# Kernel tuning notes

Measured on AMD Instinct MI355X. Metric: run time of the kernel, lower is better.

The kernel has to match this reference:

```python
import jax, jax.numpy as jnp
import numpy as np

D_MODEL = 1024
NHEAD = 16
HEAD_DIM = D_MODEL // NHEAD


def setup_inputs() -> dict:
    key = jax.random.key(0)
    k1, k2, k3 = jax.random.split(key, 3)
    x = jax.random.normal(k1, (4, 2048, D_MODEL), dtype=jnp.float32)
    # xavier_uniform init for weights, zero bias
    lim_qkv = float(np.sqrt(6.0 / (D_MODEL + 3 * D_MODEL)))
    w_qkv = jax.random.uniform(k2, (3 * D_MODEL, D_MODEL), jnp.float32, -lim_qkv, lim_qkv)
    b_qkv = jnp.zeros((3 * D_MODEL,), jnp.float32)
    lim_o = float(np.sqrt(6.0 / (D_MODEL + D_MODEL)))
    w_o = jax.random.uniform(k3, (D_MODEL, D_MODEL), jnp.float32, -lim_o, lim_o)
    b_o = jnp.zeros((D_MODEL,), jnp.float32)
    return {"x": x, "w_qkv": w_qkv, "b_qkv": b_qkv, "w_o": w_o, "b_o": b_o}


def reference(x, w_qkv, b_qkv, w_o, b_o):
    B, S, _ = x.shape
    qkv = x @ w_qkv.T + b_qkv                      # [B,S,3D]
    qkv = qkv.reshape(B, S, NHEAD, 3 * HEAD_DIM).transpose(0, 2, 1, 3)  # [B,H,S,3d]
    q, k, v = jnp.split(qkv, 3, axis=-1)           # each [B,H,S,d]
    scale = 1.0 / jnp.sqrt(jnp.asarray(HEAD_DIM, x.dtype))
    logits = jnp.einsum('bhqd,bhkd->bhqk', q, k) * scale
    attn = jax.nn.softmax(logits, axis=-1)
    vals = jnp.einsum('bhqk,bhkd->bhqd', attn, v)  # [B,H,S,d]
    vals = vals.transpose(0, 2, 1, 3).reshape(B, S, D_MODEL)
    return vals @ w_o.T + b_o
```

## Files before the change

kernel.cpp:

```cpp
#include <hip/hip_runtime.h>
#include <hip/hip_bf16.h>
#include <stdint.h>

typedef unsigned short u16;
typedef __bf16 bf16x8 __attribute__((ext_vector_type(8)));
typedef short s16x4 __attribute__((ext_vector_type(4)));
typedef float f32x4 __attribute__((ext_vector_type(4)));
typedef u16 u16x4v __attribute__((ext_vector_type(4)));

#define AS1 __attribute__((address_space(1)))
#define AS3 __attribute__((address_space(3)))

__device__ __forceinline__ void gld_lds16(const u16* g, u16* l) {
    __builtin_amdgcn_global_load_lds((const AS1 uint32_t*)g, (AS3 uint32_t*)l, 16, 0, 0);
}

__device__ __forceinline__ u16 f2bf(float f) {
    union { float f; uint32_t u; } v; v.f = f;
    uint32_t u = v.u;
    return (u16)((u + 0x7FFFu + ((u >> 16) & 1u)) >> 16);
}

#define QSCALE 0.18033688011112042f

__global__ void cast_f32_bf16(const float* __restrict__ in, u16* __restrict__ out, int n4) {
    int i = blockIdx.x * blockDim.x + threadIdx.x;
    if (i < n4) {
        float4 f = ((const float4*)in)[i];
        u16x4v o;
        o.x = f2bf(f.x); o.y = f2bf(f.y); o.z = f2bf(f.z); o.w = f2bf(f.w);
        ((u16x4v*)out)[i] = o;
    }
}

template <int MODE>
__global__ __launch_bounds__(256, 2) void gemm_bt(
    const u16* __restrict__ A, const u16* __restrict__ B,
    const float* __restrict__ bias, float* __restrict__ Cf,
    u16* __restrict__ qb, u16* __restrict__ kb, u16* __restrict__ vT,
    int K, int ldc)
{
    __shared__ __align__(16) u16 As[128 * 32];
    __shared__ __align__(16) u16 Bs[128 * 32];
    const int tid = threadIdx.x;
    const int lane = tid & 63;
    const int w = tid >> 6;
    const int wm = (w >> 1) << 6;
    const int wn = (w & 1) << 6;
    const int r = lane & 15;
    const int q = lane >> 4;
    const int m0 = blockIdx.y << 7;
    const int n0 = blockIdx.x << 7;

    const f32x4 zero4 = {0.f, 0.f, 0.f, 0.f};
    f32x4 acc[4][4];
#pragma unroll
    for (int i = 0; i < 4; ++i)
#pragma unroll
        for (int j = 0; j < 4; ++j) acc[i][j] = zero4;

    const int nk = K >> 5;
    for (int kt = 0; kt < nk; ++kt) {
        const int kk = kt << 5;
#pragma unroll
        for (int p = 0; p < 2; ++p) {
            const int idx = (p << 8) + tid;
            const int row = idx >> 2;
            const int cg = ((idx & 3) - (row >> 1)) & 3;
            gld_lds16(A + (m0 + row) * K + kk + (cg << 3), &As[idx << 3]);
            gld_lds16(B + (n0 + row) * K + kk + (cg << 3), &Bs[idx << 3]);
        }
        __syncthreads();
        bf16x8 af[4], bf[4];
#pragma unroll
        for (int i = 0; i < 4; ++i) {
            const int ra = wm + (i << 4) + r;
            af[i] = *(const bf16x8*)&As[((ra << 2) + ((q + (ra >> 1)) & 3)) << 3];
            const int rb = wn + (i << 4) + r;
            bf[i] = *(const bf16x8*)&Bs[((rb << 2) + ((q + (rb >> 1)) & 3)) << 3];
        }
#pragma unroll
        for (int i = 0; i < 4; ++i)
#pragma unroll
            for (int j = 0; j < 4; ++j)
                acc[i][j] = __builtin_amdgcn_mfma_f32_16x16x32_bf16(af[i], bf[j], acc[i][j], 0, 0, 0);
        __syncthreads();
    }

#pragma unroll
    for (int j = 0; j < 4; ++j) {
        const int col = n0 + wn + (j << 4) + r;
        const float bv = bias[col];
        if (MODE == 0) {
#pragma unroll
            for (int i = 0; i < 4; ++i)
#pragma unroll
                for (int ii = 0; ii < 4; ++ii) {
                    const int rowg = m0 + wm + (i << 4) + (q << 2) + ii;
                    Cf[rowg * ldc + col] = acc[i][j][ii] + bv;
                }
        } else {
            const int c0 = n0 + wn + (j << 4);
            const int h = c0 / 192;
            const int rem = c0 - h * 192;
            const int region = rem >> 6;
            const int colp = (h << 6) + (rem - (region << 6)) + r;
            if (region == 0) {
#pragma unroll
                for (int i = 0; i < 4; ++i)
#pragma unroll
                    for (int ii = 0; ii < 4; ++ii) {
                        const int rowg = m0 + wm + (i << 4) + (q << 2) + ii;
                        qb[rowg * 1024 + colp] = f2bf((acc[i][j][ii] + bv) * QSCALE);
                    }
            } else if (region == 1) {
#pragma unroll
                for (int i = 0; i < 4; ++i)
#pragma unroll
                    for (int ii = 0; ii < 4; ++ii) {
                        const int rowg = m0 + wm + (i << 4) + (q << 2) + ii;
                        kb[rowg * 1024 + colp] = f2bf(acc[i][j][ii] + bv);
                    }
            } else {
#pragma unroll
                for (int i = 0; i < 4; ++i) {
                    const int rowg0 = m0 + wm + (i << 4) + (q << 2);
                    u16x4v vv;
                    vv.x = f2bf(acc[i][j][0] + bv);
                    vv.y = f2bf(acc[i][j][1] + bv);
                    vv.z = f2bf(acc[i][j][2] + bv);
                    vv.w = f2bf(acc[i][j][3] + bv);
                    *(u16x4v*)&vT[(size_t)colp * 8192 + rowg0] = vv;
                }
            }
        }
    }
}

__device__ __forceinline__ void stage_kv(
    const u16* __restrict__ kb, const u16* __restrict__ vT, u16* __restrict__ KV,
    int tid, int h, size_t rowbase, int k0)
{
#pragma unroll
    for (int p = 0; p < 2; ++p) {
        const int idx = (p << 8) + tid;
        const int row = idx >> 3;
        const int cg = ((idx & 7) - row) & 7;
        gld_lds16(kb + (rowbase + k0 + row) * 1024 + (h << 6) + (cg << 3), &KV[idx << 3]);
    }
#pragma unroll
    for (int p = 0; p < 2; ++p) {
        const int idx = (p << 8) + tid;
        const int hd = idx >> 3;
        const int pc = idx & 7;
        const int lc = (pc - hd - (hd >> 3)) & 7;
        gld_lds16(vT + (size_t)((h << 6) + hd) * 8192 + rowbase + k0 + (lc << 3),
                  &KV[4096 + (idx << 3)]);
    }
}

__global__ __launch_bounds__(256, 3) void attn(
    const u16* __restrict__ qb, const u16* __restrict__ kb,
    const u16* __restrict__ vT, u16* __restrict__ vals)
{
    __shared__ __align__(16) u16 S[16384];

    const int tid = threadIdx.x;
    const int lane = tid & 63;
    const int w = tid >> 6;
    const int r = lane & 15;
    const int q = lane >> 4;
    const int h = blockIdx.x;
    const int q0 = blockIdx.y << 7;
    const int b = blockIdx.z;
    const size_t rowbase = (size_t)b * 2048;

#pragma unroll
    for (int p = 0; p < 4; ++p) {
        const int idx = (p << 8) + tid;
        const int row = idx >> 3;
        const int cg = ((idx & 7) - row) & 7;
        gld_lds16(qb + (rowbase + q0 + row) * 1024 + (h << 6) + (cg << 3), &S[idx << 3]);
    }
    stage_kv(kb, vT, S + 8192, tid, h, rowbase, 0);
    __syncthreads();

    bf16x8 bq[2][2];
#pragma unroll
    for (int ks = 0; ks < 2; ++ks) {
        const int L = (ks << 2) + q;
#pragma unroll
        for (int nt = 0; nt < 2; ++nt) {
            const int row = (w << 5) + (nt << 4) + r;
            bq[ks][nt] = *(const bf16x8*)&S[(row << 6) + (((L + row) & 7) << 3)];
        }
    }
    __syncthreads();

    const f32x4 zero4 = {0.f, 0.f, 0.f, 0.f};
    f32x4 oacc[4][2];
    f32x4 lacc[2];
#pragma unroll
    for (int ht = 0; ht < 4; ++ht)
#pragma unroll
        for (int nt = 0; nt < 2; ++nt) oacc[ht][nt] = zero4;
    lacc[0] = zero4; lacc[1] = zero4;

    const s16x4 ones = {0x3F80, 0x3F80, 0x3F80, 0x3F80};

    for (int kt = 0; kt < 32; ++kt) {
        const int cur = kt & 1;
        if (kt > 0) __syncthreads();
        u16* bufP = (cur == 0) ? (S + 0) : (S + 8192);
        const u16* bufC = (cur == 0) ? (S + 8192) : (S + 0);
        if (kt < 31) stage_kv(kb, vT, bufP, tid, h, rowbase, (kt + 1) << 6);
        const u16* Ks = bufC;
        const u16* VTs = bufC + 4096;

        f32x4 sacc[4][2];
#pragma unroll
        for (int mt = 0; mt < 4; ++mt)
#pragma unroll
            for (int nt = 0; nt < 2; ++nt) sacc[mt][nt] = zero4;
#pragma unroll
        for (int ks = 0; ks < 2; ++ks) {
            const int L = (ks << 2) + q;
            bf16x8 ak[4];
#pragma unroll
            for (int mt = 0; mt < 4; ++mt) {
                const int row = (mt << 4) + r;
                ak[mt] = *(const bf16x8*)&Ks[(row << 6) + (((L + row) & 7) << 3)];
            }
#pragma unroll
            for (int mt = 0; mt < 4; ++mt)
#pragma unroll
                for (int nt = 0; nt < 2; ++nt)
                    sacc[mt][nt] = __builtin_amdgcn_mfma_f32_16x16x32_bf16(ak[mt], bq[ks][nt], sacc[mt][nt], 0, 0, 0);
        }

        s16x4 pb[4][2];
#pragma unroll
        for (int mt = 0; mt < 4; ++mt) {
#pragma unroll
            for (int nt = 0; nt < 2; ++nt) {
                const float e0 = __builtin_amdgcn_exp2f(sacc[mt][nt][0]);
                const float e1 = __builtin_amdgcn_exp2f(sacc[mt][nt][1]);
                const float e2 = __builtin_amdgcn_exp2f(sacc[mt][nt][2]);
                const float e3 = __builtin_amdgcn_exp2f(sacc[mt][nt][3]);
                union { __hip_bfloat162 h2[2]; s16x4 v; } u;
                u.h2[0] = __float22bfloat162_rn(float2{e0, e1});
                u.h2[1] = __float22bfloat162_rn(float2{e2, e3});
                pb[mt][nt] = u.v;
                lacc[nt] = __builtin_amdgcn_mfma_f32_16x16x16bf16_1k(ones, pb[mt][nt], lacc[nt], 0, 0, 0);
            }
        }

#pragma unroll
        for (int mt = 0; mt < 4; ++mt) {
            s16x4 av[4];
#pragma unroll
            for (int ht = 0; ht < 4; ++ht) {
                const int hd = (ht << 4) + r;
                const int chunk = (mt << 1) + (q >> 1);
                const int pc = (chunk + hd + (hd >> 3)) & 7;
                av[ht] = *(const s16x4*)&VTs[(hd << 6) + (pc << 3) + ((q & 1) << 2)];
            }
#pragma unroll
            for (int ht = 0; ht < 4; ++ht)
#pragma unroll
                for (int nt = 0; nt < 2; ++nt)
                    oacc[ht][nt] = __builtin_amdgcn_mfma_f32_16x16x16bf16_1k(av[ht], pb[mt][nt], oacc[ht][nt], 0, 0, 0);
        }
    }

#pragma unroll
    for (int nt = 0; nt < 2; ++nt) {
        const float inv = 1.f / lacc[nt][0];
        const int srow = q0 + (w << 5) + (nt << 4) + r;
#pragma unroll
        for (int ht = 0; ht < 4; ++ht) {
            u16x4v vv;
            vv.x = f2bf(oacc[ht][nt][0] * inv);
            vv.y = f2bf(oacc[ht][nt][1] * inv);
            vv.z = f2bf(oacc[ht][nt][2] * inv);
            vv.w = f2bf(oacc[ht][nt][3] * inv);
            const int col = (h << 6) + (ht << 4) + (q << 2);
            *(u16x4v*)&vals[(rowbase + srow) * 1024 + col] = vv;
        }
    }
}

extern "C" void kernel_launch(void* const* d_in, const int* in_sizes, int n_in,
                              void* d_out, int out_size, void* d_ws, size_t ws_size,
                              hipStream_t stream) {
    (void)in_sizes; (void)n_in; (void)out_size; (void)ws_size;
    const float* x     = (const float*)d_in[0];
    const float* w_qkv = (const float*)d_in[1];
    const float* b_qkv = (const float*)d_in[2];
    const float* w_o   = (const float*)d_in[3];
    const float* b_o   = (const float*)d_in[4];
    float* out = (float*)d_out;

    char* ws = (char*)d_ws;
    u16* xb    = (u16*)(ws);
    u16* wqkvb = (u16*)(ws + (size_t)(16 << 20));
    u16* wob   = (u16*)(ws + (size_t)(22 << 20));
    u16* qb    = (u16*)(ws + (size_t)(24 << 20));
    u16* kb    = (u16*)(ws + (size_t)(40 << 20));
    u16* vTb   = (u16*)(ws + (size_t)(56 << 20));
    u16* valsb = (u16*)(ws + (size_t)(72 << 20));

    cast_f32_bf16<<<8192, 256, 0, stream>>>(x, xb, 2097152);
    cast_f32_bf16<<<3072, 256, 0, stream>>>(w_qkv, wqkvb, 786432);
    cast_f32_bf16<<<1024, 256, 0, stream>>>(w_o, wob, 262144);

    gemm_bt<1><<<dim3(24, 64), 256, 0, stream>>>(xb, wqkvb, b_qkv, nullptr,
                                                 qb, kb, vTb, 1024, 3072);

    attn<<<dim3(16, 16, 4), 256, 0, stream>>>(qb, kb, vTb, valsb);

    gemm_bt<0><<<dim3(8, 64), 256, 0, stream>>>(valsb, wob, b_o, out,
                                                nullptr, nullptr, nullptr, 1024, 1024);
}
```

Baseline: 278.0 us.

## Switch attention to 32x32x16 MFMA with permlane32 swap and XOR-swizzled LDS

Rewrites the attention inner loop to use 32x32x16 bf16 MFMA tiles instead of 16x16 tiles. The exponentiated scores are repacked into the B-operand layout with v_permlane32_swap, so they feed the PV MFMA straight from registers. The change also swaps the additive LDS swizzle for an XOR swizzle with precomputed staging pointers, and wraps the MFMA blocks in s_setprio. The aim is fewer MFMA issues, fewer LDS reads and less address arithmetic per tile. The cost is higher register pressure and a dependency on the MI355 permlane32_swap instruction.

New measurement: 291.3 us. 1.05x slower.

```diff
diff --git a/kernel.cpp b/kernel.cpp
--- a/kernel.cpp
+++ b/kernel.cpp
@@ -3,10 +3,12 @@
 #include <stdint.h>
 
 typedef unsigned short u16;
+typedef uint32_t u32;
 typedef __bf16 bf16x8 __attribute__((ext_vector_type(8)));
-typedef short s16x4 __attribute__((ext_vector_type(4)));
 typedef float f32x4 __attribute__((ext_vector_type(4)));
+typedef float f32x16 __attribute__((ext_vector_type(16)));
 typedef u16 u16x4v __attribute__((ext_vector_type(4)));
+typedef u32 u32x2 __attribute__((ext_vector_type(2)));
 
 #define AS1 __attribute__((address_space(1)))
 #define AS3 __attribute__((address_space(3)))
@@ -19,6 +21,15 @@
     union { float f; uint32_t u; } v; v.f = f;
     uint32_t u = v.u;
     return (u16)((u + 0x7FFFu + ((u >> 16) & 1u)) >> 16);
+}
+
+__device__ __forceinline__ u32x2 pl32swap(u32 a, u32 b) {
+#if __has_builtin(__builtin_amdgcn_permlane32_swap)
+    return __builtin_amdgcn_permlane32_swap(a, b, false, false);
+#else
+    asm volatile("v_permlane32_swap_b32 %0, %1" : "+v"(a), "+v"(b));
+    u32x2 r; r[0] = a; r[1] = b; return r;
+#endif
 }
 
 #define QSCALE 0.18033688011112042f
@@ -137,157 +148,149 @@
     }
 }
 
-__device__ __forceinline__ void stage_kv(
-    const u16* __restrict__ kb, const u16* __restrict__ vT, u16* __restrict__ KV,
-    int tid, int h, size_t rowbase, int k0)
-{
-#pragma unroll
-    for (int p = 0; p < 2; ++p) {
-        const int idx = (p << 8) + tid;
-        const int row = idx >> 3;
-        const int cg = ((idx & 7) - row) & 7;
-        gld_lds16(kb + (rowbase + k0 + row) * 1024 + (h << 6) + (cg << 3), &KV[idx << 3]);
-    }
-#pragma unroll
-    for (int p = 0; p < 2; ++p) {
-        const int idx = (p << 8) + tid;
-        const int hd = idx >> 3;
-        const int pc = idx & 7;
-        const int lc = (pc - hd - (hd >> 3)) & 7;
-        gld_lds16(vT + (size_t)((h << 6) + hd) * 8192 + rowbase + k0 + (lc << 3),
-                  &KV[4096 + (idx << 3)]);
-    }
-}
-
 __global__ __launch_bounds__(256, 3) void attn(
     const u16* __restrict__ qb, const u16* __restrict__ kb,
     const u16* __restrict__ vT, u16* __restrict__ vals)
 {
     __shared__ __align__(16) u16 S[16384];
 
-    const int tid = threadIdx.x;
+    const int tid  = threadIdx.x;
     const int lane = tid & 63;
-    const int w = tid >> 6;
-    const int r = lane & 15;
-    const int q = lane >> 4;
-    const int h = blockIdx.x;
-    const int q0 = blockIdx.y << 7;
-    const int b = blockIdx.z;
+    const int w    = tid >> 6;
+    const int c    = lane & 31;
+    const int h2   = lane >> 5;
+    const int head = blockIdx.x;
+    const int q0   = blockIdx.y << 7;
+    const int b    = blockIdx.z;
     const size_t rowbase = (size_t)b * 2048;
 
 #pragma unroll
     for (int p = 0; p < 4; ++p) {
         const int idx = (p << 8) + tid;
         const int row = idx >> 3;
-        const int cg = ((idx & 7) - row) & 7;
-        gld_lds16(qb + (rowbase + q0 + row) * 1024 + (h << 6) + (cg << 3), &S[idx << 3]);
-    }
-    stage_kv(kb, vT, S + 8192, tid, h, rowbase, 0);
+        const int cg  = (idx & 7) ^ (row & 7);
+        gld_lds16(qb + (rowbase + q0 + row) * 1024 + (head << 6) + (cg << 3), &S[idx << 3]);
+    }
+
+    const int srow8 = tid >> 3;
+    const int scg   = (tid & 7) ^ (srow8 & 7);
+    const u16* gK = kb + (rowbase + srow8) * 1024 + (head << 6) + (scg << 3);
+    const u16* gV = vT + (size_t)((head << 6) + srow8) * 8192 + rowbase + (scg << 3);
+
+    {
+        u16* buf = S + 8192;
+        gld_lds16(gK,             &buf[tid << 3]);
+        gld_lds16(gK + 32 * 1024, &buf[2048 + (tid << 3)]);
+        gld_lds16(gV,             &buf[4096 + (tid << 3)]);
+        gld_lds16(gV + 32 * 8192, &buf[6144 + (tid << 3)]);
+    }
     __syncthreads();
 
-    bf16x8 bq[2][2];
-#pragma unroll
-    for (int ks = 0; ks < 2; ++ks) {
-        const int L = (ks << 2) + q;
-#pragma unroll
-        for (int nt = 0; nt < 2; ++nt) {
-            const int row = (w << 5) + (nt << 4) + r;
-            bq[ks][nt] = *(const bf16x8*)&S[(row << 6) + (((L + row) & 7) << 3)];
-        }
+    const int qrow = (w << 5) + c;
+    bf16x8 bq[4];
+#pragma unroll
+    for (int dc = 0; dc < 4; ++dc) {
+        const int L = (dc << 1) + h2;
+        bq[dc] = *(const bf16x8*)&S[(qrow << 6) + ((L ^ (c & 7)) << 3)];
     }
     __syncthreads();
 
-    const f32x4 zero4 = {0.f, 0.f, 0.f, 0.f};
-    f32x4 oacc[4][2];
-    f32x4 lacc[2];
-#pragma unroll
-    for (int ht = 0; ht < 4; ++ht)
-#pragma unroll
-        for (int nt = 0; nt < 2; ++nt) oacc[ht][nt] = zero4;
-    lacc[0] = zero4; lacc[1] = zero4;
-
-    const s16x4 ones = {0x3F80, 0x3F80, 0x3F80, 0x3F80};
+    const int ldsb = (c << 6) + ((h2 ^ (c & 7)) << 3);
+
+    f32x16 oacc[2], lacc;
+#pragma unroll
+    for (int i = 0; i < 16; ++i) { oacc[0][i] = 0.f; oacc[1][i] = 0.f; lacc[i] = 0.f; }
+
+    union { u16 u[8]; bf16x8 v; } Ou;
+#pragma unroll
+    for (int i = 0; i < 8; ++i) Ou.u[i] = 0x3F80;
+    const bf16x8 ones8 = Ou.v;
+
+    const u16* gKr = gK + 65536;
+    const u16* gVr = gV + 64;
 
     for (int kt = 0; kt < 32; ++kt) {
         const int cur = kt & 1;
         if (kt > 0) __syncthreads();
         u16* bufP = (cur == 0) ? (S + 0) : (S + 8192);
         const u16* bufC = (cur == 0) ? (S + 8192) : (S + 0);
-        if (kt < 31) stage_kv(kb, vT, bufP, tid, h, rowbase, (kt + 1) << 6);
-        const u16* Ks = bufC;
+        if (kt < 31) {
+            gld_lds16(gKr,             &bufP[tid << 3]);
+            gld_lds16(gKr + 32 * 1024, &bufP[2048 + (tid << 3)]);
+            gld_lds16(gVr,             &bufP[4096 + (tid << 3)]);
+            gld_lds16(gVr + 32 * 8192, &bufP[6144 + (tid << 3)]);
+            gKr += 65536;
+            gVr += 64;
+        }
+        const u16* Ks  = bufC;
         const u16* VTs = bufC + 4096;
 
-        f32x4 sacc[4][2];
-#pragma unroll
-        for (int mt = 0; mt < 4; ++mt)
-#pragma unroll
-            for (int nt = 0; nt < 2; ++nt) sacc[mt][nt] = zero4;
-#pragma unroll
-        for (int ks = 0; ks < 2; ++ks) {
-            const int L = (ks << 2) + q;
-            bf16x8 ak[4];
-#pragma unroll
-            for (int mt = 0; mt < 4; ++mt) {
-                const int row = (mt << 4) + r;
-                ak[mt] = *(const bf16x8*)&Ks[(row << 6) + (((L + row) & 7) << 3)];
+        f32x16 sacc[2];
+#pragma unroll
+        for (int i = 0; i < 16; ++i) { sacc[0][i] = 0.f; sacc[1][i] = 0.f; }
+        __builtin_amdgcn_s_setprio(1);
+#pragma unroll
+        for (int mt = 0; mt < 2; ++mt)
+#pragma unroll
+            for (int dc = 0; dc < 4; ++dc) {
+                const bf16x8 ak = *(const bf16x8*)&Ks[ldsb ^ ((mt << 11) | (dc << 4))];
+                sacc[mt] = __builtin_amdgcn_mfma_f32_32x32x16_bf16(ak, bq[dc], sacc[mt], 0, 0, 0);
             }
-#pragma unroll
-            for (int mt = 0; mt < 4; ++mt)
-#pragma unroll
-                for (int nt = 0; nt < 2; ++nt)
-                    sacc[mt][nt] = __builtin_amdgcn_mfma_f32_16x16x32_bf16(ak[mt], bq[ks][nt], sacc[mt][nt], 0, 0, 0);
-        }
-
-        s16x4 pb[4][2];
-#pragma unroll
-        for (int mt = 0; mt < 4; ++mt) {
-#pragma unroll
-            for (int nt = 0; nt < 2; ++nt) {
-                const float e0 = __builtin_amdgcn_exp2f(sacc[mt][nt][0]);
-                const float e1 = __builtin_amdgcn_exp2f(sacc[mt][nt][1]);
-                const float e2 = __builtin_amdgcn_exp2f(sacc[mt][nt][2]);
-                const float e3 = __builtin_amdgcn_exp2f(sacc[mt][nt][3]);
-                union { __hip_bfloat162 h2[2]; s16x4 v; } u;
-                u.h2[0] = __float22bfloat162_rn(float2{e0, e1});
-                u.h2[1] = __float22bfloat162_rn(float2{e2, e3});
-                pb[mt][nt] = u.v;
-                lacc[nt] = __builtin_amdgcn_mfma_f32_16x16x16bf16_1k(ones, pb[mt][nt], lacc[nt], 0, 0, 0);
+        __builtin_amdgcn_s_setprio(0);
+
+#pragma unroll
+        for (int mt = 0; mt < 2; ++mt) {
+            bf16x8 av[4];
+#pragma unroll
+            for (int ht = 0; ht < 2; ++ht)
+#pragma unroll
+                for (int c16 = 0; c16 < 2; ++c16)
+                    av[(ht << 1) | c16] =
+                        *(const bf16x8*)&VTs[ldsb ^ ((ht << 11) | (mt << 5) | (c16 << 4))];
+
+            u32 pk[8];
+#pragma unroll
+            for (int p = 0; p < 8; ++p) {
+                const float e0 = __builtin_amdgcn_exp2f(sacc[mt][2 * p]);
+                const float e1 = __builtin_amdgcn_exp2f(sacc[mt][2 * p + 1]);
+                union { __hip_bfloat162 h; u32 d; } u;
+                u.h = __float22bfloat162_rn(float2{e0, e1});
+                pk[p] = u.d;
             }
-        }
-
-#pragma unroll
-        for (int mt = 0; mt < 4; ++mt) {
-            s16x4 av[4];
-#pragma unroll
-            for (int ht = 0; ht < 4; ++ht) {
-                const int hd = (ht << 4) + r;
-                const int chunk = (mt << 1) + (q >> 1);
-                const int pc = (chunk + hd + (hd >> 3)) & 7;
-                av[ht] = *(const s16x4*)&VTs[(hd << 6) + (pc << 3) + ((q & 1) << 2)];
+            const u32x2 r02 = pl32swap(pk[0], pk[2]);
+            const u32x2 r13 = pl32swap(pk[1], pk[3]);
+            const u32x2 r46 = pl32swap(pk[4], pk[6]);
+            const u32x2 r57 = pl32swap(pk[5], pk[7]);
+            union { u32 d[4]; bf16x8 v; } A0, A1;
+            A0.d[0] = r02[0]; A0.d[1] = r13[0]; A0.d[2] = r02[1]; A0.d[3] = r13[1];
+            A1.d[0] = r46[0]; A1.d[1] = r57[0]; A1.d[2] = r46[1]; A1.d[3] = r57[1];
+
+            __builtin_amdgcn_s_setprio(1);
+            lacc = __builtin_amdgcn_mfma_f32_32x32x16_bf16(ones8, A0.v, lacc, 0, 0, 0);
+            lacc = __builtin_amdgcn_mfma_f32_32x32x16_bf16(ones8, A1.v, lacc, 0, 0, 0);
+#pragma unroll
+            for (int ht = 0; ht < 2; ++ht) {
+                oacc[ht] = __builtin_amdgcn_mfma_f32_32x32x16_bf16(av[(ht << 1) | 0], A0.v, oacc[ht], 0, 0, 0);
+                oacc[ht] = __builtin_amdgcn_mfma_f32_32x32x16_bf16(av[(ht << 1) | 1], A1.v, oacc[ht], 0, 0, 0);
             }
-#pragma unroll
-            for (int ht = 0; ht < 4; ++ht)
-#pragma unroll
-                for (int nt = 0; nt < 2; ++nt)
-                    oacc[ht][nt] = __builtin_amdgcn_mfma_f32_16x16x16bf16_1k(av[ht], pb[mt][nt], oacc[ht][nt], 0, 0, 0);
-        }
-    }
-
-#pragma unroll
-    for (int nt = 0; nt < 2; ++nt) {
-        const float inv = 1.f / lacc[nt][0];
-        const int srow = q0 + (w << 5) + (nt << 4) + r;
-#pragma unroll
-        for (int ht = 0; ht < 4; ++ht) {
+            __builtin_amdgcn_s_setprio(0);
+        }
+    }
+
+    const float inv = 1.f / lacc[0];
+    const size_t orow = rowbase + q0 + (w << 5) + c;
+#pragma unroll
+    for (int ht = 0; ht < 2; ++ht)
+#pragma unroll
+        for (int r4 = 0; r4 < 4; ++r4) {
             u16x4v vv;
-            vv.x = f2bf(oacc[ht][nt][0] * inv);
-            vv.y = f2bf(oacc[ht][nt][1] * inv);
-            vv.z = f2bf(oacc[ht][nt][2] * inv);
-            vv.w = f2bf(oacc[ht][nt][3] * inv);
-            const int col = (h << 6) + (ht << 4) + (q << 2);
-            *(u16x4v*)&vals[(rowbase + srow) * 1024 + col] = vv;
-        }
-    }
+            vv.x = f2bf(oacc[ht][4 * r4 + 0] * inv);
+            vv.y = f2bf(oacc[ht][4 * r4 + 1] * inv);
+            vv.z = f2bf(oacc[ht][4 * r4 + 2] * inv);
+            vv.w = f2bf(oacc[ht][4 * r4 + 3] * inv);
+            const int hd0 = (ht << 5) + (r4 << 3) + (h2 << 2);
+            *(u16x4v*)&vals[orow * 1024 + (head << 6) + hd0] = vv;
+        }
 }
 
 extern "C" void kernel_launch(void* const* d_in, const int* in_sizes, int n_in,
```
